# Kernel optimization log

Measured on AMD Instinct MI355X. Metric: run time of the kernel, lower is better.

The kernel has to match this reference:

```python
import jax, jax.numpy as jnp
import numpy as np

N = 4096      # nodes
F = 64        # feature dim (= in = hidden = out channels)
DEPTH = 3
RATIO = 0.5


def _gcn(x, A, W, b):
    # GCNConv(improved=True): self-loop weight 2.0, sym-normalized propagation
    n = A.shape[0]
    A_hat = A + 2.0 * jnp.eye(n, dtype=A.dtype)
    deg = A_hat.sum(axis=1)
    dinv = jnp.where(deg > 0, jax.lax.rsqrt(deg), 0.0)
    A_norm = dinv[:, None] * A_hat * dinv[None, :]
    return A_norm @ (x @ W) + b


def _augment(A):
    # add_self_loops (fill 1.0) -> spspmm(A,A) -> remove_self_loops, dense form
    n = A.shape[0]
    eye = jnp.eye(n, dtype=A.dtype)
    A_sl = A + eye
    A2 = A_sl @ A_sl
    return A2 * (1.0 - eye)


def _topk_pool(x, A, p, ratio):
    # TopKPooling: score = tanh((x @ p)/||p||); keep top ceil(ratio*N) nodes
    score = jnp.tanh((x @ p) / jnp.linalg.norm(p))
    k = int(np.ceil(ratio * x.shape[0]))          # static
    vals, perm = jax.lax.top_k(score, k)
    x_new = x[perm] * vals[:, None]
    A_new = A[perm][:, perm]                      # filter_adj
    return x_new, A_new, perm


def setup_inputs() -> dict:
    key = jax.random.key(0)
    ks = jax.random.split(key, 9)
    x = jax.random.normal(ks[0], (N, F), dtype=jnp.float32)
    # sparse random undirected graph, avg degree ~32, no self loops
    u = jax.random.uniform(ks[1], (N, N), dtype=jnp.float32)
    m = (u < (16.0 / N)).astype(jnp.float32)
    adj = jnp.maximum(m, m.T) * (1.0 - jnp.eye(N, dtype=jnp.float32))
    s = 1.0 / np.sqrt(F)
    down_W = jax.random.normal(ks[2], (DEPTH + 1, F, F), dtype=jnp.float32) * s
    down_b = jnp.zeros((DEPTH + 1, F), dtype=jnp.float32)
    pool_w = jax.random.normal(ks[3], (DEPTH, F), dtype=jnp.float32) * s
    up_W = jax.random.normal(ks[4], (DEPTH, F, F), dtype=jnp.float32) * s
    up_b = jnp.zeros((DEPTH, F), dtype=jnp.float32)
    fc_w = jax.random.normal(ks[5], (F, 1), dtype=jnp.float32) * s
    fc_b = jnp.zeros((1,), dtype=jnp.float32)
    prob = jnp.zeros((), dtype=jnp.float32)  # dropout p = 0 -> deterministic
    return {"x": x, "adj": adj, "prob": prob, "down_W": down_W,
            "down_b": down_b, "pool_w": pool_w, "up_W": up_W,
            "up_b": up_b, "fc_w": fc_w, "fc_b": fc_b}


def reference(x, adj, prob, down_W, down_b, pool_w, up_W, up_b, fc_w, fc_b):
    act = jax.nn.relu
    A = adj
    h = act(_gcn(x, A, down_W[0], down_b[0]))
    xs, As, perms = [h], [A], []
    for i in range(DEPTH):
        A = _augment(A)
        h, A, perm = _topk_pool(h, A, pool_w[i], RATIO)
        h = act(_gcn(h, A, down_W[i + 1], down_b[i + 1]))
        if i < DEPTH - 1:
            xs.append(h); As.append(A)
        perms.append(perm)
    for i in range(DEPTH):
        j = DEPTH - 1 - i
        res, A, perm = xs[j], As[j], perms[j]
        up = jnp.zeros_like(res).at[perm].set(h)   # scatter unpool
        h = res + up                               # sum_res
        h = _gcn(h, A, up_W[i], up_b[i])
        if i < DEPTH - 1:
            h = act(h)
    h = jax.nn.relu(h)
    h = h / (1.0 - prob)   # dropout with p=prob(=0): all-ones keep mask
    return h @ fc_w + fc_b
```

## Files before the change

### kernel.cpp

```cpp
#include <hip/hip_runtime.h>
#include <cstdint>
#include <cstddef>


typedef float  f4v    __attribute__((ext_vector_type(4)));
typedef float  f32x4  __attribute__((ext_vector_type(4)));
typedef __bf16 bf16x8 __attribute__((ext_vector_type(8)));
typedef __bf16 bf16x4 __attribute__((ext_vector_type(4)));
typedef int    i32x4  __attribute__((ext_vector_type(4)));

#define NN0 4096
#define NN1 2048
#define NN2 1024
#define NN3 512

__global__ __launch_bounds__(256) void k_zs_deg(const float* __restrict__ X,
                                                const float* __restrict__ W,
                                                const float* __restrict__ A,
                                                int n,
                                                float* __restrict__ DEG,
                                                float* __restrict__ zs,
                                                __bf16* __restrict__ ADJB,
                                                __bf16* __restrict__ Zt0,
                                                __bf16* __restrict__ Zt1,
                                                __bf16* __restrict__ Zt2) {
    __shared__ float Ws[64][65];
    __shared__ float Xs[4][64];
    __shared__ float degs[4];
    int tid = threadIdx.x;
#pragma unroll
    for (int q = 0; q < 16; q++) {
        int idx = q * 256 + tid;
        Ws[idx >> 6][idx & 63] = W[idx];
    }
    int row0 = blockIdx.x << 2;
    int r = tid >> 6, lane = tid & 63;
    const float* ar = A + (size_t)(row0 + r) * n;
    __bf16* ab = ADJB + (size_t)(row0 + r) * n;
    float s = 0.f;
    for (int j = lane << 2; j < n; j += 256) {
        f4v a = *(const f4v*)(ar + j);
        s += a[0] + a[1] + a[2] + a[3];
        bf16x4 b;
#pragma unroll
        for (int e = 0; e < 4; e++) b[e] = (__bf16)a[e];
        *(bf16x4*)(ab + j) = b;
    }
#pragma unroll
    for (int off = 32; off > 0; off >>= 1) s += __shfl_xor(s, off);
    if (lane == 0) { degs[r] = s; DEG[row0 + r] = s; }
    Xs[r][lane] = X[((size_t)(row0 + r) << 6) + lane];
    __syncthreads();
    float acc = 0.f;
#pragma unroll
    for (int k = 0; k < 64; k++) acc = fmaf(Xs[r][k], Ws[k][lane], acc);
    float di = 1.0f / sqrtf(degs[r] + 2.0f);
    float zval = di * acc;
    zs[((size_t)(row0 + r) << 6) + lane] = zval;
    __syncthreads();
    Xs[r][lane] = zval;
    __syncthreads();
    int c = tid >> 2, rr = tid & 3;
    float v = Xs[rr][c];
    float v0 = (float)(__bf16)v;
    float v1 = (float)(__bf16)(v - v0);
    size_t o = (size_t)c * n + row0 + rr;
    Zt0[o] = (__bf16)v0;
    Zt1[o] = (__bf16)(v - v0);
    Zt2[o] = (__bf16)(v - v0 - v1);
}

__global__ __launch_bounds__(256) void k_zs_pool(const float* __restrict__ H,
                                                 const float* __restrict__ sc,
                                                 const int* __restrict__ perm,
                                                 const float* __restrict__ W,
                                                 const float* __restrict__ deg,
                                                 float* __restrict__ zs,
                                                 __bf16* __restrict__ Zt0,
                                                 __bf16* __restrict__ Zt1,
                                                 __bf16* __restrict__ Zt2,
                                                 int n) {
    __shared__ float Ws[64][65];
    __shared__ float Xs[4][64];
    int tid = threadIdx.x;
#pragma unroll
    for (int q = 0; q < 16; q++) {
        int idx = q * 256 + tid;
        Ws[idx >> 6][idx & 63] = W[idx];
    }
    int row0 = blockIdx.x << 2;
    int r = tid >> 6, f = tid & 63;
    int src = perm[row0 + r];
    Xs[r][f] = H[((size_t)src << 6) + f] * sc[src];
    __syncthreads();
    float acc = 0.f;
#pragma unroll
    for (int k = 0; k < 64; k++) acc = fmaf(Xs[r][k], Ws[k][f], acc);
    float di = 1.0f / sqrtf(deg[row0 + r] + 2.0f);
    float zval = di * acc;
    zs[((size_t)(row0 + r) << 6) + f] = zval;
    if (Zt0) {
        __syncthreads();
        Xs[r][f] = zval;
        __syncthreads();
        int c = tid >> 2, rr = tid & 3;
        float v = Xs[rr][c];
        float v0 = (float)(__bf16)v;
        float v1 = (float)(__bf16)(v - v0);
        size_t o = (size_t)c * n + row0 + rr;
        Zt0[o] = (__bf16)v0;
        Zt1[o] = (__bf16)(v - v0);
        if (Zt2) Zt2[o] = (__bf16)(v - v0 - v1);
    }
}

__global__ __launch_bounds__(256) void k_zs_unpool(const float* __restrict__ RES,
                                                   const float* __restrict__ HS,
                                                   const int* __restrict__ inv,
                                                   const float* __restrict__ W,
                                                   const float* __restrict__ deg,
                                                   float* __restrict__ zs,
                                                   __bf16* __restrict__ Zt0,
                                                   __bf16* __restrict__ Zt1,
                                                   __bf16* __restrict__ Zt2,
                                                   int n) {
    __shared__ float Ws[64][65];
    __shared__ float Xs[4][64];
    int tid = threadIdx.x;
#pragma unroll
    for (int q = 0; q < 16; q++) {
        int idx = q * 256 + tid;
        Ws[idx >> 6][idx & 63] = W[idx];
    }
    int row0 = blockIdx.x << 2;
    int r = tid >> 6, f = tid & 63;
    int grow = row0 + r;
    int iv = inv[grow];
    float xv = RES[((size_t)grow << 6) + f];
    if (iv >= 0) xv += HS[((size_t)iv << 6) + f];
    Xs[r][f] = xv;
    __syncthreads();
    float acc = 0.f;
#pragma unroll
    for (int k = 0; k < 64; k++) acc = fmaf(Xs[r][k], Ws[k][f], acc);
    float di = 1.0f / sqrtf(deg[grow] + 2.0f);
    float zval = di * acc;
    zs[((size_t)grow << 6) + f] = zval;
    if (Zt0) {
        __syncthreads();
        Xs[r][f] = zval;
        __syncthreads();
        int c = tid >> 2, rr = tid & 3;
        float v = Xs[rr][c];
        float v0 = (float)(__bf16)v;
        float v1 = (float)(__bf16)(v - v0);
        size_t o = (size_t)c * n + row0 + rr;
        Zt0[o] = (__bf16)v0;
        Zt1[o] = (__bf16)(v - v0);
        if (Zt2) Zt2[o] = (__bf16)(v - v0 - v1);
    }
}

__global__ __launch_bounds__(256) void k_prop(const float* __restrict__ A,
                                              const float* __restrict__ zs,
                                              float* __restrict__ ypart,
                                              int n, int chunk) {
    int rb = blockIdx.x;
    int j0 = blockIdx.y * chunk;
    __shared__ float AtT[64][68];
    __shared__ float Zt[64][68];
    int tid = threadIdx.x;
    int lr = tid >> 2;
    int lc = (tid & 3) << 4;
    int ty = tid >> 4, tx = tid & 15;
    float acc[4][4] = {};
    const float* Arow = A + (size_t)(rb * 64 + lr) * n;
    for (int jt = j0; jt < j0 + chunk; jt += 64) {
#pragma unroll
        for (int q = 0; q < 4; q++) {
            f4v av = *(const f4v*)(Arow + jt + lc + (q << 2));
#pragma unroll
            for (int e = 0; e < 4; e++) AtT[lc + (q << 2) + e][lr] = av[e];
        }
#pragma unroll
        for (int q = 0; q < 4; q++) {
            f4v zv = *(const f4v*)(zs + (((size_t)(jt + lr)) << 6) + lc + (q << 2));
            *(f4v*)&Zt[lr][lc + (q << 2)] = zv;
        }
        __syncthreads();
#pragma unroll 4
        for (int k = 0; k < 64; k++) {
            f4v a4 = *(const f4v*)&AtT[k][ty << 2];
            f4v z4 = *(const f4v*)&Zt[k][tx << 2];
#pragma unroll
            for (int r = 0; r < 4; r++)
#pragma unroll
                for (int c = 0; c < 4; c++)
                    acc[r][c] = fmaf(a4[r], z4[c], acc[r][c]);
        }
        __syncthreads();
    }
    float* yp = ypart + ((size_t)blockIdx.y * n << 6);
#pragma unroll
    for (int r = 0; r < 4; r++) {
        f4v o; o[0] = acc[r][0]; o[1] = acc[r][1]; o[2] = acc[r][2]; o[3] = acc[r][3];
        *(f4v*)(yp + (((size_t)(rb * 64 + (ty << 2) + r)) << 6) + (tx << 2)) = o;
    }
}

template<int NP>
__global__ __launch_bounds__(256) void k_propm(const __bf16* __restrict__ Zt0,
                                               const __bf16* __restrict__ Zt1,
                                               const __bf16* __restrict__ Zt2,
                                               const __bf16* __restrict__ Ab,
                                               float* __restrict__ ypart,
                                               int n, int chunk) {
    __shared__ __bf16 At[128 * 64];
    __shared__ __bf16 B[NP][64 * 64];
    const __bf16* Zp[3] = {Zt0, Zt1, Zt2};
    int tid = threadIdx.x;
    int m0 = blockIdx.x * 128;
    int k0b = blockIdx.y * chunk;
    int wave = tid >> 6, lane = tid & 63, quad = lane >> 4, l16 = lane & 15;
    int wm = wave << 5;
    f32x4 acc[2][4] = {};
    for (int k0 = k0b; k0 < k0b + chunk; k0 += 64) {
#pragma unroll
        for (int it = 0; it < 4; it++) {
            int e = it * 256 + tid;
            int row = e >> 3, seg = e & 7;
            int sg = seg ^ (row & 7);
            const __bf16* g = Ab + ((size_t)(m0 + row) * n + k0 + (sg << 3));
            __builtin_amdgcn_global_load_lds(
                (const __attribute__((address_space(1))) void*)g,
                (__attribute__((address_space(3))) void*)(At + (e << 3)), 16, 0, 0);
        }
#pragma unroll
        for (int it = 0; it < 2; it++) {
            int e = it * 256 + tid;
            int row = e >> 3, seg = e & 7;
            int sg = seg ^ (row & 7);
            size_t off = (size_t)row * n + k0 + (sg << 3);
#pragma unroll
            for (int p = 0; p < NP; p++)
                __builtin_amdgcn_global_load_lds(
                    (const __attribute__((address_space(1))) void*)(Zp[p] + off),
                    (__attribute__((address_space(3))) void*)(B[p] + (e << 3)), 16, 0, 0);
        }
        __syncthreads();
#pragma unroll
        for (int kk = 0; kk < 2; kk++) {
            int s = (kk << 2) + quad;
            bf16x8 af[2];
#pragma unroll
            for (int im = 0; im < 2; im++) {
                int row = wm + (im << 4) + l16;
                af[im] = *(const bf16x8*)(At + (row << 6) + ((s ^ (row & 7)) << 3));
            }
#pragma unroll
            for (int cg = 0; cg < 4; cg++) {
                int brow = (cg << 4) + l16;
                int so = (s ^ (brow & 7)) << 3;
#pragma unroll
                for (int p = 0; p < NP; p++) {
                    bf16x8 bv = *(const bf16x8*)(B[p] + (brow << 6) + so);
#pragma unroll
                    for (int im = 0; im < 2; im++)
                        acc[im][cg] = __builtin_amdgcn_mfma_f32_16x16x32_bf16(
                            af[im], bv, acc[im][cg], 0, 0, 0);
                }
            }
        }
        __syncthreads();
    }
    float* yp = ypart + ((size_t)blockIdx.y * n << 6);
#pragma unroll
    for (int im = 0; im < 2; im++)
#pragma unroll
        for (int cg = 0; cg < 4; cg++)
#pragma unroll
            for (int r = 0; r < 4; r++) {
                int grow = m0 + wm + (im << 4) + (quad << 2) + r;
                int gcol = (cg << 4) + l16;
                yp[((size_t)grow << 6) + gcol] = acc[im][cg][r];
            }
}

__global__ __launch_bounds__(256) void k_epi(const float* __restrict__ ypart,
                                             const float* __restrict__ zs,
                                             const float* __restrict__ deg,
                                             const float* __restrict__ b,
                                             float* __restrict__ H, int n, int S,
                                             int relu,
                                             const float* __restrict__ p,
                                             float* __restrict__ score,
                                             int* __restrict__ cnt,
                                             const float* __restrict__ fcw,
                                             const float* __restrict__ fcb,
                                             const float* __restrict__ prob,
                                             float* __restrict__ out) {
    int idx = blockIdx.x * 256 + threadIdx.x;
    int i = idx >> 6, f = idx & 63;
    size_t stride = (size_t)n << 6;
    float y = 0.f;
    for (int s2 = 0; s2 < S; s2++) y += ypart[(size_t)s2 * stride + idx];
    float di = 1.0f / sqrtf(deg[i] + 2.0f);
    float v = di * (y + 2.0f * zs[idx]) + b[f];
    if (relu) v = fmaxf(v, 0.f);
    if (H) H[idx] = v;
    if (p) {
        float pv = p[f];
        float d = v * pv, q = pv * pv;
#pragma unroll
        for (int off = 32; off > 0; off >>= 1) {
            d += __shfl_xor(d, off);
            q += __shfl_xor(q, off);
        }
        if (f == 0) score[i] = tanhf(d / sqrtf(q));
        if (idx < n) cnt[idx] = 0;
    }
    if (fcw) {
        float hv = fmaxf(v, 0.f) * fcw[f];
#pragma unroll
        for (int off = 32; off > 0; off >>= 1) hv += __shfl_xor(hv, off);
        if (f == 0) out[i] = hv / (1.0f - prob[0]) + fcb[0];
    }
}

__global__ __launch_bounds__(256) void k_topk_count(const float* __restrict__ score,
                                                    int* __restrict__ cnt, int n) {
    __shared__ float sc[256];
    int j0 = blockIdx.y * 256;
    sc[threadIdx.x] = score[j0 + threadIdx.x];
    int i = blockIdx.x * 256 + threadIdx.x;
    float si = score[i];
    __syncthreads();
    int c = 0;
#pragma unroll 8
    for (int t = 0; t < 256; t++) {
        float sj = sc[t];
        int j = j0 + t;
        c += ((sj > si) || (sj == si && j < i)) ? 1 : 0;
    }
    atomicAdd(&cnt[i], c);
}
__global__ __launch_bounds__(256) void k_topk_scatter(const int* __restrict__ cnt,
                                                      int* __restrict__ perm,
                                                      int* __restrict__ inv,
                                                      float* __restrict__ degN,
                                                      int k) {
    int i = blockIdx.x * 256 + threadIdx.x;
    int c = cnt[i];
    if (c < k) perm[c] = i;
    inv[i] = (c < k) ? c : -1;
    if (i < k) degN[i] = 0.f;
}

__global__ __launch_bounds__(256) void k_gather8b(const __bf16* __restrict__ Ab,
                                                  const int* __restrict__ perm,
                                                  signed char* __restrict__ Mg,
                                                  int kbits4 ) {
    size_t idx16 = (size_t)blockIdx.x * 256 + threadIdx.x;
    int r = (int)(idx16 >> kbits4);
    int c = ((int)idx16 & ((1 << kbits4) - 1)) << 4;
    int K = 1 << (kbits4 + 4);
    int src = perm[r];
    const __bf16* rowp = Ab + (size_t)src * K + c;
    bf16x8 a0 = *(const bf16x8*)rowp;
    bf16x8 a1 = *(const bf16x8*)(rowp + 8);
    union { signed char ch[16]; i32x4 v; } u;
#pragma unroll
    for (int j = 0; j < 8; j++) {
        float val = (float)a0[j];
        if (src == c + j) val += 1.0f;
        u.ch[j] = (signed char)val;
    }
#pragma unroll
    for (int j = 0; j < 8; j++) {
        float val = (float)a1[j];
        if (src == c + 8 + j) val += 1.0f;
        u.ch[8 + j] = (signed char)val;
    }
    *(i32x4*)(Mg + (idx16 << 4)) = u.v;
}

__global__ __launch_bounds__(256) void k_gather(const float* __restrict__ A,
                                                const int* __restrict__ perm,
                                                __bf16* __restrict__ Mg,
                                                int kbits3 ) {
    size_t idx8 = (size_t)blockIdx.x * 256 + threadIdx.x;
    int r = (int)(idx8 >> kbits3);
    int c = ((int)idx8 & ((1 << kbits3) - 1)) << 3;
    int K = 1 << (kbits3 + 3);
    int src = perm[r];
    const float* rowp = A + (size_t)src * K + c;
    f4v v0 = *(const f4v*)rowp;
    f4v v1 = *(const f4v*)(rowp + 4);
    bf16x8 t;
#pragma unroll
    for (int j = 0; j < 4; j++) {
        float v = v0[j]; if (src == c + j) v += 1.0f; t[j] = (__bf16)v;
    }
#pragma unroll
    for (int j = 0; j < 4; j++) {
        float v = v1[j]; if (src == c + 4 + j) v += 1.0f; t[4 + j] = (__bf16)v;
    }
    *(bf16x8*)(Mg + idx8 * 8) = t;
}

template<int BN>
__global__ __launch_bounds__(256) void k_augmm_i8(const signed char* __restrict__ Mg,
                                                  float* __restrict__ C,
                                                  __bf16* __restrict__ Cb,
                                                  float* __restrict__ DEG,
                                                  int nk, int K) {
    __shared__ signed char At[64 * 128];
    __shared__ signed char Bt[BN * 128];
    constexpr int NI = BN / 32;
    int tid = threadIdx.x;
    int m0 = blockIdx.x * 64, n0 = blockIdx.y * BN;
    int wave = tid >> 6, lane = tid & 63;
    int wm = (wave >> 1) << 5;
    int wn = (wave & 1) * (BN >> 1);
    int quad = lane >> 4, l16 = lane & 15;
    i32x4 acc[2][NI] = {};
    for (int k0 = 0; k0 < K; k0 += 128) {
#pragma unroll
        for (int it = 0; it < 2; it++) {
            int e = it * 256 + tid;
            int row = e >> 3, cs = e & 7;
            int cg = cs ^ (row & 7);
            const signed char* g = Mg + ((size_t)(m0 + row) * K + k0 + (cg << 4));
            __builtin_amdgcn_global_load_lds(
                (const __attribute__((address_space(1))) void*)g,
                (__attribute__((address_space(3))) void*)(At + (e << 4)), 16, 0, 0);
        }
#pragma unroll
        for (int it = 0; it < BN / 32; it++) {
            int e = it * 256 + tid;
            int row = e >> 3, cs = e & 7;
            int cg = cs ^ (row & 7);
            const signed char* g = Mg + ((size_t)(n0 + row) * K + k0 + (cg << 4));
            __builtin_amdgcn_global_load_lds(
                (const __attribute__((address_space(1))) void*)g,
                (__attribute__((address_space(3))) void*)(Bt + (e << 4)), 16, 0, 0);
        }
        __syncthreads();
#pragma unroll
        for (int h = 0; h < 2; h++) {
            int cix = (h << 2) + quad;
            i32x4 af[2], bf[NI];
#pragma unroll
            for (int im = 0; im < 2; im++) {
                int row = wm + (im << 4) + l16;
                af[im] = *(const i32x4*)(At + (row << 7) + ((cix ^ (row & 7)) << 4));
            }
#pragma unroll
            for (int in2 = 0; in2 < NI; in2++) {
                int row = wn + (in2 << 4) + l16;
                bf[in2] = *(const i32x4*)(Bt + (row << 7) + ((cix ^ (row & 7)) << 4));
            }
#pragma unroll
            for (int im = 0; im < 2; im++)
#pragma unroll
                for (int in2 = 0; in2 < NI; in2++)
                    acc[im][in2] = __builtin_amdgcn_mfma_i32_16x16x64_i8(
                        af[im], bf[in2], acc[im][in2], 0, 0, 0);
        }
        __syncthreads();
    }
#pragma unroll
    for (int im = 0; im < 2; im++) {
#pragma unroll
        for (int r = 0; r < 4; r++) {
            int grow = m0 + wm + (im << 4) + (quad << 2) + r;
            int part = 0;
#pragma unroll
            for (int in2 = 0; in2 < NI; in2++) {
                int gcol = n0 + wn + (in2 << 4) + l16;
                int v = (grow == gcol) ? 0 : acc[im][in2][r];
                if (C)  C[(size_t)grow * nk + gcol] = (float)v;
                if (Cb) Cb[(size_t)grow * nk + gcol] = (__bf16)(float)v;
                part += v;
            }
#pragma unroll
            for (int off = 8; off > 0; off >>= 1) part += __shfl_xor(part, off);
            if (l16 == 0) atomicAdd(&DEG[grow], (float)part);
        }
    }
}

__global__ __launch_bounds__(256) void k_augmm_bf(const __bf16* __restrict__ Mg,
                                                  float* __restrict__ C,
                                                  float* __restrict__ DEG,
                                                  int nk, int K) {
    constexpr int BN = 64;
    __shared__ __bf16 At[64 * 64];
    __shared__ __bf16 Bt[BN * 64];
    constexpr int NI = BN / 32;
    int tid = threadIdx.x;
    int m0 = blockIdx.x * 64, n0 = blockIdx.y * BN;
    int wave = tid >> 6, lane = tid & 63;
    int wm = (wave >> 1) << 5;
    int wn = (wave & 1) * (BN >> 1);
    int quad = lane >> 4, l16 = lane & 15;
    f32x4 acc[2][NI] = {};
    for (int k0 = 0; k0 < K; k0 += 64) {
#pragma unroll
        for (int it = 0; it < 2; it++) {
            int e = it * 256 + tid;
            int row = e >> 3, seg = e & 7;
            int sg = seg ^ (row & 7);
            const __bf16* g = Mg + ((size_t)(m0 + row) * K + k0 + (sg << 3));
            __builtin_amdgcn_global_load_lds(
                (const __attribute__((address_space(1))) void*)g,
                (__attribute__((address_space(3))) void*)(At + (e << 3)), 16, 0, 0);
        }
#pragma unroll
        for (int it = 0; it < BN / 32; it++) {
            int e = it * 256 + tid;
            int row = e >> 3, seg = e & 7;
            int sg = seg ^ (row & 7);
            const __bf16* g = Mg + ((size_t)(n0 + row) * K + k0 + (sg << 3));
            __builtin_amdgcn_global_load_lds(
                (const __attribute__((address_space(1))) void*)g,
                (__attribute__((address_space(3))) void*)(Bt + (e << 3)), 16, 0, 0);
        }
        __syncthreads();
#pragma unroll
        for (int kk = 0; kk < 2; kk++) {
            int s = (kk << 2) + quad;
            bf16x8 af[2], bfm[NI];
#pragma unroll
            for (int im = 0; im < 2; im++) {
                int row = wm + (im << 4) + l16;
                af[im] = *(const bf16x8*)(At + (row << 6) + ((s ^ (row & 7)) << 3));
            }
#pragma unroll
            for (int in2 = 0; in2 < NI; in2++) {
                int row = wn + (in2 << 4) + l16;
                bfm[in2] = *(const bf16x8*)(Bt + (row << 6) + ((s ^ (row & 7)) << 3));
            }
#pragma unroll
            for (int im = 0; im < 2; im++)
#pragma unroll
                for (int in2 = 0; in2 < NI; in2++)
                    acc[im][in2] = __builtin_amdgcn_mfma_f32_16x16x32_bf16(
                        af[im], bfm[in2], acc[im][in2], 0, 0, 0);
        }
        __syncthreads();
    }
#pragma unroll
    for (int im = 0; im < 2; im++) {
#pragma unroll
        for (int r = 0; r < 4; r++) {
            int grow = m0 + wm + (im << 4) + (quad << 2) + r;
            float part = 0.f;
#pragma unroll
            for (int in2 = 0; in2 < NI; in2++) {
                int gcol = n0 + wn + (in2 << 4) + l16;
                float v = (grow == gcol) ? 0.f : acc[im][in2][r];
                C[(size_t)grow * nk + gcol] = v;
                part += v;
            }
#pragma unroll
            for (int off = 8; off > 0; off >>= 1) part += __shfl_xor(part, off);
            if (l16 == 0) atomicAdd(&DEG[grow], part);
        }
    }
}

extern "C" void kernel_launch(void* const* d_in, const int* in_sizes, int n_in,
                              void* d_out, int out_size, void* d_ws, size_t ws_size,
                              hipStream_t stream) {
    (void)in_sizes; (void)n_in; (void)out_size;
    const float* x     = (const float*)d_in[0];
    const float* adj   = (const float*)d_in[1];
    const float* prob  = (const float*)d_in[2];
    const float* downW = (const float*)d_in[3];
    const float* downb = (const float*)d_in[4];
    const float* poolw = (const float*)d_in[5];
    const float* upW   = (const float*)d_in[6];
    const float* upb   = (const float*)d_in[7];
    const float* fcw   = (const float*)d_in[8];
    const float* fcb   = (const float*)d_in[9];

    char* ws = (char*)d_ws;
    signed char* MG8 = (signed char*)(ws + 0);
    __bf16* MGB  = (__bf16*)(ws + 0);
    float*  A2   = (float*)(ws + 25165824);
    float*  A3   = (float*)(ws + 29360128);
    __bf16* ADJB = (__bf16*)(ws + 30408704);
    __bf16* A1B  = (__bf16*)(ws + 63963136);
    float*  H0   = (float*)(ws + 72351744);
    float*  H1   = (float*)(ws + 73400320);
    float*  H2   = (float*)(ws + 73924608);
    float*  H3   = (float*)(ws + 74186752);
    float*  ZS   = (float*)(ws + 74317824);
    __bf16* ZT0  = (__bf16*)(ws + 75366400);
    __bf16* ZT1  = (__bf16*)(ws + 75890688);
    __bf16* ZT2  = (__bf16*)(ws + 76414976);
    float*  YP   = (float*)(ws + 76939264);
    float*  UA   = (float*)(ws + 93716480);
    float*  UB   = (float*)(ws + 94240768);
    float*  DEG0 = (float*)(ws + 94765056);
    float*  DEG1 = (float*)(ws + 94781440);
    float*  DEG2 = (float*)(ws + 94789632);
    float*  DEG3 = (float*)(ws + 94793728);
    float*  SCORE= (float*)(ws + 94795776);
    int*    PERM0= (int*)(ws + 94812160);
    int*    PERM1= (int*)(ws + 94820352);
    int*    PERM2= (int*)(ws + 94824448);
    int*    INV0 = (int*)(ws + 94826496);
    int*    INV1 = (int*)(ws + 94842880);
    int*    INV2 = (int*)(ws + 94851072);
    int*    CNT  = (int*)(ws + 94855168);
    if (ws_size < (size_t)94871552) return;

    k_zs_deg<<<NN0 / 4, 256, 0, stream>>>(x, downW, adj, NN0, DEG0, ZS,
                                          ADJB, ZT0, ZT1, ZT2);
    k_propm<3><<<dim3(NN0 / 128, 16), 256, 0, stream>>>(ZT0, ZT1, ZT2, ADJB, YP, NN0, 256);
    k_epi<<<NN0 / 4, 256, 0, stream>>>(YP, ZS, DEG0, downb, H0, NN0, 16, 1,
                                       poolw + 0, SCORE, CNT,
                                       nullptr, nullptr, nullptr, nullptr);
    k_topk_count<<<dim3(NN0 / 256, NN0 / 256), 256, 0, stream>>>(SCORE, CNT, NN0);
    k_topk_scatter<<<NN0 / 256, 256, 0, stream>>>(CNT, PERM0, INV0, DEG1, NN1);
    k_gather8b<<<(NN1 * NN0 / 16) / 256, 256, 0, stream>>>(ADJB, PERM0, MG8, 8);
    k_augmm_i8<128><<<dim3(NN1 / 64, NN1 / 128), 256, 0, stream>>>(MG8, nullptr, A1B, DEG1, NN1, NN0);
    k_zs_pool<<<NN1 / 4, 256, 0, stream>>>(H0, SCORE, PERM0, downW + 4096, DEG1, ZS,
                                           ZT0, ZT1, ZT2, NN1);
    k_propm<3><<<dim3(NN1 / 128, 32), 256, 0, stream>>>(ZT0, ZT1, ZT2, A1B, YP, NN1, 64);
    k_epi<<<NN1 / 4, 256, 0, stream>>>(YP, ZS, DEG1, downb + 64, H1, NN1, 32, 1,
                                       poolw + 64, SCORE, CNT,
                                       nullptr, nullptr, nullptr, nullptr);
    k_topk_count<<<dim3(NN1 / 256, NN1 / 256), 256, 0, stream>>>(SCORE, CNT, NN1);
    k_topk_scatter<<<NN1 / 256, 256, 0, stream>>>(CNT, PERM1, INV1, DEG2, NN2);
    k_gather8b<<<(NN2 * NN1 / 16) / 256, 256, 0, stream>>>(A1B, PERM1, MG8, 7);
    k_augmm_i8<64><<<dim3(NN2 / 64, NN2 / 64), 256, 0, stream>>>(MG8, A2, nullptr, DEG2, NN2, NN1);
    k_zs_pool<<<NN2 / 4, 256, 0, stream>>>(H1, SCORE, PERM1, downW + 2 * 4096, DEG2, ZS,
                                           nullptr, nullptr, nullptr, NN2);
    k_prop<<<dim3(NN2 / 64, 16), 256, 0, stream>>>(A2, ZS, YP, NN2, 64);
    k_epi<<<NN2 / 4, 256, 0, stream>>>(YP, ZS, DEG2, downb + 2 * 64, H2, NN2, 16, 1,
                                       poolw + 128, SCORE, CNT,
                                       nullptr, nullptr, nullptr, nullptr);
    k_topk_count<<<dim3(NN2 / 256, NN2 / 256), 256, 0, stream>>>(SCORE, CNT, NN2);
    k_topk_scatter<<<NN2 / 256, 256, 0, stream>>>(CNT, PERM2, INV2, DEG3, NN3);
    k_gather<<<(NN3 * NN2 / 8) / 256, 256, 0, stream>>>(A2, PERM2, MGB, 7);
    k_augmm_bf<<<dim3(NN3 / 64, NN3 / 64), 256, 0, stream>>>(MGB, A3, DEG3, NN3, NN2);
    k_zs_pool<<<NN3 / 4, 256, 0, stream>>>(H2, SCORE, PERM2, downW + 3 * 4096, DEG3, ZS,
                                           nullptr, nullptr, nullptr, NN3);
    k_prop<<<dim3(NN3 / 64, 8), 256, 0, stream>>>(A3, ZS, YP, NN3, 64);
    k_epi<<<NN3 / 4, 256, 0, stream>>>(YP, ZS, DEG3, downb + 3 * 64, H3, NN3, 8, 1,
                                       nullptr, nullptr, nullptr,
                                       nullptr, nullptr, nullptr, nullptr);

    k_zs_unpool<<<NN2 / 4, 256, 0, stream>>>(H2, H3, INV2, upW, DEG2, ZS,
                                             nullptr, nullptr, nullptr, NN2);
    k_prop<<<dim3(NN2 / 64, 16), 256, 0, stream>>>(A2, ZS, YP, NN2, 64);
    k_epi<<<NN2 / 4, 256, 0, stream>>>(YP, ZS, DEG2, upb, UA, NN2, 16, 1,
                                       nullptr, nullptr, nullptr,
                                       nullptr, nullptr, nullptr, nullptr);
    k_zs_unpool<<<NN1 / 4, 256, 0, stream>>>(H1, UA, INV1, upW + 4096, DEG1, ZS,
                                             ZT0, ZT1, nullptr, NN1);
    k_propm<2><<<dim3(NN1 / 128, 32), 256, 0, stream>>>(ZT0, ZT1, nullptr, A1B, YP, NN1, 64);
    k_epi<<<NN1 / 4, 256, 0, stream>>>(YP, ZS, DEG1, upb + 64, UB, NN1, 32, 1,
                                       nullptr, nullptr, nullptr,
                                       nullptr, nullptr, nullptr, nullptr);
    k_zs_unpool<<<NN0 / 4, 256, 0, stream>>>(H0, UB, INV0, upW + 2 * 4096, DEG0, ZS,
                                             ZT0, ZT1, nullptr, NN0);
    k_propm<2><<<dim3(NN0 / 128, 16), 256, 0, stream>>>(ZT0, ZT1, nullptr, ADJB, YP, NN0, 256);
    k_epi<<<NN0 / 4, 256, 0, stream>>>(YP, ZS, DEG0, upb + 2 * 64, nullptr, NN0, 16, 0,
                                       nullptr, nullptr, nullptr,
                                       fcw, fcb, prob, (float*)d_out);
}
```

Before: 357.6 us.

## Replace first-level dense A² augmentation with sparse neighbor-list row expansion

During the first degree pass, each row's nonzero column indices are recorded into a fixed 128-slot neighbor list. The dense gather plus int8 matmul that computed (A+I)² restricted to kept rows is replaced by a per-row kernel. That kernel walks neighbors-of-neighbors and accumulates counts in LDS with atomics, then writes the bf16 row and its degree. This trades a 2048x2048x4096 dense matmul for sparse work proportional to degree squared. It assumes no row has more than 128 neighbors and depends on the LDS atomic path being cheap.

```diff
diff --git a/kernel.cpp b/kernel.cpp
--- a/kernel.cpp
+++ b/kernel.cpp
@@ -21,22 +21,29 @@
                                                 float* __restrict__ DEG,
                                                 float* __restrict__ zs,
                                                 __bf16* __restrict__ ADJB,
+                                                int* __restrict__ NBR,
+                                                int* __restrict__ NCNT,
                                                 __bf16* __restrict__ Zt0,
                                                 __bf16* __restrict__ Zt1,
                                                 __bf16* __restrict__ Zt2) {
     __shared__ float Ws[64][65];
     __shared__ float Xs[4][64];
     __shared__ float degs[4];
+    __shared__ int lcnt[4];
     int tid = threadIdx.x;
 #pragma unroll
     for (int q = 0; q < 16; q++) {
         int idx = q * 256 + tid;
         Ws[idx >> 6][idx & 63] = W[idx];
     }
+    if (tid < 4) lcnt[tid] = 0;
+    __syncthreads();
     int row0 = blockIdx.x << 2;
     int r = tid >> 6, lane = tid & 63;
-    const float* ar = A + (size_t)(row0 + r) * n;
-    __bf16* ab = ADJB + (size_t)(row0 + r) * n;
+    int grow = row0 + r;
+    const float* ar = A + (size_t)grow * n;
+    __bf16* ab = ADJB + (size_t)grow * n;
+    int* nbr = NBR + ((size_t)grow << 7);
     float s = 0.f;
     for (int j = lane << 2; j < n; j += 256) {
         f4v a = *(const f4v*)(ar + j);
@@ -45,18 +52,24 @@
 #pragma unroll
         for (int e = 0; e < 4; e++) b[e] = (__bf16)a[e];
         *(bf16x4*)(ab + j) = b;
+#pragma unroll
+        for (int e = 0; e < 4; e++)
+            if (a[e] != 0.0f) {
+                int slot = atomicAdd(&lcnt[r], 1);
+                nbr[slot] = j + e;
+            }
     }
 #pragma unroll
     for (int off = 32; off > 0; off >>= 1) s += __shfl_xor(s, off);
-    if (lane == 0) { degs[r] = s; DEG[row0 + r] = s; }
-    Xs[r][lane] = X[((size_t)(row0 + r) << 6) + lane];
+    if (lane == 0) { degs[r] = s; DEG[grow] = s; NCNT[grow] = lcnt[r]; }
+    Xs[r][lane] = X[((size_t)grow << 6) + lane];
     __syncthreads();
     float acc = 0.f;
 #pragma unroll
     for (int k = 0; k < 64; k++) acc = fmaf(Xs[r][k], Ws[k][lane], acc);
     float di = 1.0f / sqrtf(degs[r] + 2.0f);
     float zval = di * acc;
-    zs[((size_t)(row0 + r) << 6) + lane] = zval;
+    zs[((size_t)grow << 6) + lane] = zval;
     __syncthreads();
     Xs[r][lane] = zval;
     __syncthreads();
@@ -354,6 +367,50 @@
     if (c < k) perm[c] = i;
     inv[i] = (c < k) ? c : -1;
     if (i < k) degN[i] = 0.f;
+}
+
+__global__ __launch_bounds__(256) void k_rowaug(const int* __restrict__ NBR,
+                                                const int* __restrict__ NCNT,
+                                                const int* __restrict__ perm,
+                                                const int* __restrict__ inv,
+                                                __bf16* __restrict__ Cb,
+                                                float* __restrict__ DEG,
+                                                int nk) {
+    __shared__ int Crow[4][2048];
+    int wave = threadIdx.x >> 6, lane = threadIdx.x & 63;
+    int a = (blockIdx.x << 2) + wave;
+    int* cr = Crow[wave];
+    for (int b = lane; b < nk; b += 64) cr[b] = 0;
+    int pa = perm[a];
+    int cnt_a = NCNT[pa];
+    const int* nbrA = NBR + ((size_t)pa << 7);
+    int v0 = nbrA[lane];
+    int v1 = nbrA[64 + lane];
+    for (int ka = 0; ka <= cnt_a; ka++) {
+        int k = (ka == cnt_a) ? pa
+                              : ((ka < 64) ? __shfl(v0, ka) : __shfl(v1, ka - 64));
+        int ck = NCNT[k];
+        const int* nk2 = NBR + ((size_t)k << 7);
+        for (int t = lane; t < ck; t += 64) {
+            int iu = inv[nk2[t]];
+            if (iu >= 0) atomicAdd(&cr[iu], 1);
+        }
+        if (lane == 0) {
+            int iu = inv[k];
+            if (iu >= 0) atomicAdd(&cr[iu], 1);
+        }
+    }
+    float s = 0.f;
+    __bf16* crow_out = Cb + (size_t)a * nk;
+    for (int b = lane; b < nk; b += 64) {
+        int v = cr[b];
+        if (b == a) v = 0;
+        crow_out[b] = (__bf16)(float)v;
+        s += (float)v;
+    }
+#pragma unroll
+    for (int off = 32; off > 0; off >>= 1) s += __shfl_xor(s, off);
+    if (lane == 0) DEG[a] = s;
 }
 
 __global__ __launch_bounds__(256) void k_gather8b(const __bf16* __restrict__ Ab,
@@ -615,18 +672,19 @@
     int*    INV1 = (int*)(ws + 94842880);
     int*    INV2 = (int*)(ws + 94851072);
     int*    CNT  = (int*)(ws + 94855168);
-    if (ws_size < (size_t)94871552) return;
+    int*    NBR  = (int*)(ws + 94871552);
+    int*    NCNT = (int*)(ws + 96968704);
+    if (ws_size < (size_t)96985088) return;
 
     k_zs_deg<<<NN0 / 4, 256, 0, stream>>>(x, downW, adj, NN0, DEG0, ZS,
-                                          ADJB, ZT0, ZT1, ZT2);
+                                          ADJB, NBR, NCNT, ZT0, ZT1, ZT2);
     k_propm<3><<<dim3(NN0 / 128, 16), 256, 0, stream>>>(ZT0, ZT1, ZT2, ADJB, YP, NN0, 256);
     k_epi<<<NN0 / 4, 256, 0, stream>>>(YP, ZS, DEG0, downb, H0, NN0, 16, 1,
                                        poolw + 0, SCORE, CNT,
                                        nullptr, nullptr, nullptr, nullptr);
     k_topk_count<<<dim3(NN0 / 256, NN0 / 256), 256, 0, stream>>>(SCORE, CNT, NN0);
     k_topk_scatter<<<NN0 / 256, 256, 0, stream>>>(CNT, PERM0, INV0, DEG1, NN1);
-    k_gather8b<<<(NN1 * NN0 / 16) / 256, 256, 0, stream>>>(ADJB, PERM0, MG8, 8);
-    k_augmm_i8<128><<<dim3(NN1 / 64, NN1 / 128), 256, 0, stream>>>(MG8, nullptr, A1B, DEG1, NN1, NN0);
+    k_rowaug<<<NN1 / 4, 256, 0, stream>>>(NBR, NCNT, PERM0, INV0, A1B, DEG1, NN1);
     k_zs_pool<<<NN1 / 4, 256, 0, stream>>>(H0, SCORE, PERM0, downW + 4096, DEG1, ZS,
                                            ZT0, ZT1, ZT2, NN1);
     k_propm<3><<<dim3(NN1 / 128, 32), 256, 0, stream>>>(ZT0, ZT1, ZT2, A1B, YP, NN1, 64);
```

Measured after the change: 364.3 us. No clear change (+1.9%).
